# Optimization experiments

Measured on AMD Instinct MI355X. Metric: run time of the kernel, lower is better.

The kernel has to match this reference:

```python
import jax, jax.numpy as jnp
import numpy as np

D_MODEL = 1024
N_HEADS = 16
HEAD_DIM = D_MODEL // N_HEADS


def setup_inputs() -> dict:
    key = jax.random.key(0)
    k_x, k_q, k_k, k_v = jax.random.split(key, 4)
    B, S = 2, 2048
    x = jax.random.normal(k_x, (B, S, D_MODEL), dtype=jnp.float32)
    # nn.Linear weights stored as [out, in]; we apply x @ W.T
    scale = 1.0 / np.sqrt(D_MODEL)
    W_q = jax.random.uniform(k_q, (D_MODEL, D_MODEL), jnp.float32, -scale, scale)
    W_k = jax.random.uniform(k_k, (D_MODEL, D_MODEL), jnp.float32, -scale, scale)
    W_v = jax.random.uniform(k_v, (D_MODEL, D_MODEL), jnp.float32, -scale, scale)
    return {"x": x, "W_q": W_q, "W_k": W_k, "W_v": W_v}


def reference(x, W_q, W_k, W_v):
    B, S, D = x.shape
    H, Hd = N_HEADS, HEAD_DIM
    # QKV projections (Linear with no bias): x @ W.T
    Q = (x @ W_q.T).reshape(B, S, H, Hd).transpose(0, 2, 1, 3)  # [B,H,S,Hd]
    K = (x @ W_k.T).reshape(B, S, H, Hd).transpose(0, 2, 1, 3)
    V = (x @ W_v.T).reshape(B, S, H, Hd).transpose(0, 2, 1, 3)
    scores = jnp.einsum("bhqd,bhkd->bhqk", Q, K) / jnp.sqrt(jnp.float32(Hd))
    attn = jax.nn.softmax(scores, axis=-1)
    out = jnp.einsum("bhqk,bhkd->bhqd", attn, V)  # [B,H,S,Hd]
    return out.transpose(0, 2, 1, 3).reshape(B, S, H * Hd)
```

## Files before the change

kernel.cpp:

```cpp
#include <hip/hip_runtime.h>
#include <stdint.h>


typedef __bf16 bf16x8 __attribute__((ext_vector_type(8)));
typedef __bf16 bf16x4 __attribute__((ext_vector_type(4)));
typedef float  f32x4  __attribute__((ext_vector_type(4)));

#define D_MODEL 1024
#define SEQ     2048
#define NHEAD   16
#define HDIM    64
#define BS      4096

__device__ __forceinline__ void load_lds16(const void* g, void* lds) {
  __builtin_amdgcn_global_load_lds(
      (__attribute__((address_space(1))) void*)(uintptr_t)g,
      (__attribute__((address_space(3))) void*)(uintptr_t)lds,
      16, 0, 0);
}

#define NX4 1048576
#define NW4 262144
__global__ void cvt_all(const float* __restrict__ x,  const float* __restrict__ wq,
                        const float* __restrict__ wk, const float* __restrict__ wv,
                        __bf16* __restrict__ xb,  __bf16* __restrict__ wqb,
                        __bf16* __restrict__ wkb, __bf16* __restrict__ wvb) {
  int i = blockIdx.x * blockDim.x + threadIdx.x;
  const float* in; __bf16* out; int j;
  if (i < NX4)                { in = x;  out = xb;  j = i; }
  else if (i < NX4 + NW4)     { in = wq; out = wqb; j = i - NX4; }
  else if (i < NX4 + 2*NW4)   { in = wk; out = wkb; j = i - NX4 - NW4; }
  else                        { in = wv; out = wvb; j = i - NX4 - 2*NW4; }
  float4 v = ((const float4*)in)[j];
  bf16x4 o;
  o[0] = (__bf16)v.x; o[1] = (__bf16)v.y;
  o[2] = (__bf16)v.z; o[3] = (__bf16)v.w;
  ((bf16x4*)out)[j] = o;
}

__global__ __launch_bounds__(256) void qkv_gemm(
    const __bf16* __restrict__ X,
    const __bf16* __restrict__ Wq, const __bf16* __restrict__ Wk,
    const __bf16* __restrict__ Wv,
    __bf16* __restrict__ Qb, __bf16* __restrict__ Kb, __bf16* __restrict__ Vt) {
  __shared__ __bf16 As[128 * 32];
  __shared__ __bf16 Bs[128 * 32];

  const __bf16* W = (blockIdx.z == 0) ? Wq : (blockIdx.z == 1) ? Wk : Wv;

  const int t    = threadIdx.x;
  const int wv   = t >> 6;
  const int lane = t & 63;
  const int l15  = lane & 15;
  const int quad = lane >> 4;
  const int m0   = blockIdx.y * 128;
  const int n0   = blockIdx.x * 128;
  const int wm   = (wv >> 1) * 64;
  const int wn   = (wv & 1) * 64;

  f32x4 acc[4][4] = {};

  for (int it = 0; it < 32; ++it) {
    const int k0 = it * 32;
#pragma unroll
    for (int p = 0; p < 2; ++p) {
      const int c   = p * 256 + t;
      const int row = c >> 2;
      const int ko  = (c & 3) * 8;
      const unsigned lb = (unsigned)((p * 256 + wv * 64) * 16);
      load_lds16(X + (size_t)(m0 + row) * D_MODEL + k0 + ko, (char*)As + lb);
      load_lds16(W + (size_t)(n0 + row) * D_MODEL + k0 + ko, (char*)Bs + lb);
    }
    __syncthreads();

    bf16x8 af[4], bfb[4];
#pragma unroll
    for (int i = 0; i < 4; ++i)
      af[i] = *(const bf16x8*)&As[(wm + i * 16 + l15) * 32 + quad * 8];
#pragma unroll
    for (int j = 0; j < 4; ++j)
      bfb[j] = *(const bf16x8*)&Bs[(wn + j * 16 + l15) * 32 + quad * 8];
#pragma unroll
    for (int i = 0; i < 4; ++i)
#pragma unroll
      for (int j = 0; j < 4; ++j)
        acc[i][j] = __builtin_amdgcn_mfma_f32_16x16x32_bf16(af[i], bfb[j],
                                                            acc[i][j], 0, 0, 0);
    __syncthreads();
  }

  if (blockIdx.z != 2) {
    __bf16* Out = (blockIdx.z == 0) ? Qb : Kb;
    const float qs = (blockIdx.z == 0) ? 0.125f : 1.0f;
#pragma unroll
    for (int i = 0; i < 4; ++i) {
      const int rg = m0 + wm + i * 16 + quad * 4;
#pragma unroll
      for (int j = 0; j < 4; ++j) {
        const int cg = n0 + wn + j * 16 + l15;
#pragma unroll
        for (int r = 0; r < 4; ++r)
          Out[(size_t)(rg + r) * D_MODEL + cg] = (__bf16)(acc[i][j][r] * qs);
      }
    }
  } else {
#pragma unroll
    for (int i = 0; i < 4; ++i) {
      const int mg = m0 + wm + i * 16 + quad * 4;
#pragma unroll
      for (int j = 0; j < 4; ++j) {
        const int ng = n0 + wn + j * 16 + l15;
        bf16x4 v;
#pragma unroll
        for (int r = 0; r < 4; ++r) v[r] = (__bf16)acc[i][j][r];
        *(bf16x4*)&Vt[(size_t)ng * BS + mg] = v;
      }
    }
  }
}

__global__ __launch_bounds__(256) void attn(
    const __bf16* __restrict__ Qb, const __bf16* __restrict__ Kb,
    const __bf16* __restrict__ Vt, float* __restrict__ out) {
  __shared__ __bf16 Ks[64 * 64];
  __shared__ __bf16 Vs[64 * 64];
  __shared__ __bf16 Ps[4][32][72];

  const int t    = threadIdx.x;
  const int wv   = t >> 6;
  const int lane = t & 63;
  const int l15  = lane & 15;
  const int quad = lane >> 4;
  const int h    = blockIdx.y;
  const size_t bo = (size_t)blockIdx.z * SEQ;
  const int q0   = blockIdx.x * 128 + wv * 32;
  const int hd0  = h * HDIM;

  bf16x8 qf[2][2];
#pragma unroll
  for (int hh = 0; hh < 2; ++hh)
#pragma unroll
    for (int c = 0; c < 2; ++c)
      qf[hh][c] = *(const bf16x8*)&Qb[(bo + q0 + hh * 16 + l15) * D_MODEL +
                                      hd0 + c * 32 + quad * 8];

  float lsum[2][4] = {};
  f32x4 o_acc[2][4] = {};

  const int swz  = quad ^ (l15 & 7);
  const int swz4 = (quad + 4) ^ (l15 & 7);

  for (int kt = 0; kt < SEQ / 64; ++kt) {
    const int n0 = kt * 64;
#pragma unroll
    for (int p = 0; p < 2; ++p) {
      const int c   = p * 256 + t;
      const int row = c >> 3;
      const int cc  = (c & 7) ^ (row & 7);
      const unsigned lb = (unsigned)((p * 256 + wv * 64) * 16);
      load_lds16(Kb + (bo + n0 + row) * D_MODEL + hd0 + cc * 8, (char*)Ks + lb);
      load_lds16(Vt + (size_t)(hd0 + row) * BS + bo + n0 + cc * 8, (char*)Vs + lb);
    }
    __syncthreads();

    f32x4 s[2][4] = {};
#pragma unroll
    for (int nt = 0; nt < 4; ++nt) {
      const int r = nt * 16 + l15;
      bf16x8 kf0 = *(const bf16x8*)&Ks[(r * 8 + swz) * 8];
      bf16x8 kf1 = *(const bf16x8*)&Ks[(r * 8 + swz4) * 8];
#pragma unroll
      for (int hh = 0; hh < 2; ++hh) {
        s[hh][nt] = __builtin_amdgcn_mfma_f32_16x16x32_bf16(qf[hh][0], kf0, s[hh][nt], 0, 0, 0);
        s[hh][nt] = __builtin_amdgcn_mfma_f32_16x16x32_bf16(qf[hh][1], kf1, s[hh][nt], 0, 0, 0);
      }
    }

#pragma unroll
    for (int hh = 0; hh < 2; ++hh)
#pragma unroll
      for (int nt = 0; nt < 4; ++nt)
#pragma unroll
        for (int r = 0; r < 4; ++r) {
          float p = __expf(s[hh][nt][r]);
          lsum[hh][r] += p;
          Ps[wv][hh * 16 + quad * 4 + r][nt * 16 + l15] = (__bf16)p;
        }

#pragma unroll
    for (int tt = 0; tt < 4; ++tt) {
      const int r = tt * 16 + l15;
      bf16x8 vf0 = *(const bf16x8*)&Vs[(r * 8 + swz) * 8];
      bf16x8 vf1 = *(const bf16x8*)&Vs[(r * 8 + swz4) * 8];
#pragma unroll
      for (int hh = 0; hh < 2; ++hh) {
        bf16x8 pf0 = *(const bf16x8*)&Ps[wv][hh * 16 + l15][quad * 8];
        bf16x8 pf1 = *(const bf16x8*)&Ps[wv][hh * 16 + l15][32 + quad * 8];
        o_acc[hh][tt] = __builtin_amdgcn_mfma_f32_16x16x32_bf16(pf0, vf0, o_acc[hh][tt], 0, 0, 0);
        o_acc[hh][tt] = __builtin_amdgcn_mfma_f32_16x16x32_bf16(pf1, vf1, o_acc[hh][tt], 0, 0, 0);
      }
    }
    __syncthreads();
  }

#pragma unroll
  for (int hh = 0; hh < 2; ++hh)
#pragma unroll
    for (int r = 0; r < 4; ++r) {
      float s = lsum[hh][r];
      s += __shfl_xor(s, 1);
      s += __shfl_xor(s, 2);
      s += __shfl_xor(s, 4);
      s += __shfl_xor(s, 8);
      float inv = 1.f / s;
      const size_t row = bo + q0 + hh * 16 + quad * 4 + r;
#pragma unroll
      for (int tt = 0; tt < 4; ++tt)
        out[row * D_MODEL + hd0 + tt * 16 + l15] = o_acc[hh][tt][r] * inv;
    }
}

extern "C" void kernel_launch(void* const* d_in, const int* in_sizes, int n_in,
                              void* d_out, int out_size, void* d_ws, size_t ws_size,
                              hipStream_t stream) {
  const float* x  = (const float*)d_in[0];
  const float* Wq = (const float*)d_in[1];
  const float* Wk = (const float*)d_in[2];
  const float* Wv = (const float*)d_in[3];
  float* out = (float*)d_out;

  char* ws = (char*)d_ws;
  __bf16* xb  = (__bf16*)(ws);
  __bf16* wqb = (__bf16*)(ws + (8u  << 20));
  __bf16* wkb = (__bf16*)(ws + (10u << 20));
  __bf16* wvb = (__bf16*)(ws + (12u << 20));
  __bf16* Qbf = (__bf16*)(ws + (14u << 20));
  __bf16* Kbf = (__bf16*)(ws + (22u << 20));
  __bf16* Vt  = (__bf16*)(ws + (30u << 20));

  cvt_all<<<(NX4 + 3 * NW4) / 256, 256, 0, stream>>>(x, Wq, Wk, Wv,
                                                     xb, wqb, wkb, wvb);

  qkv_gemm<<<dim3(8, 32, 3), 256, 0, stream>>>(xb, wqb, wkb, wvb, Qbf, Kbf, Vt);

  attn<<<dim3(SEQ / 128, NHEAD, 2), 256, 0, stream>>>(Qbf, Kbf, Vt, out);
}
```

Baseline: 171.9 us.

## Keep P in registers via transposed 32x32 MFMA and permlane32 swap

Result: faster. 168.5 us (-2.0%).

```diff
diff --git a/kernel.cpp b/kernel.cpp
--- a/kernel.cpp
+++ b/kernel.cpp
@@ -5,6 +5,7 @@
 typedef __bf16 bf16x8 __attribute__((ext_vector_type(8)));
 typedef __bf16 bf16x4 __attribute__((ext_vector_type(4)));
 typedef float  f32x4  __attribute__((ext_vector_type(4)));
+typedef float  f32x16 __attribute__((ext_vector_type(16)));
 
 #define D_MODEL 1024
 #define SEQ     2048
@@ -124,31 +125,24 @@
     const __bf16* __restrict__ Vt, float* __restrict__ out) {
   __shared__ __bf16 Ks[64 * 64];
   __shared__ __bf16 Vs[64 * 64];
-  __shared__ __bf16 Ps[4][32][72];
 
   const int t    = threadIdx.x;
   const int wv   = t >> 6;
   const int lane = t & 63;
-  const int l15  = lane & 15;
-  const int quad = lane >> 4;
+  const int l31  = lane & 31;
+  const int half = lane >> 5;
   const int h    = blockIdx.y;
   const size_t bo = (size_t)blockIdx.z * SEQ;
   const int q0   = blockIdx.x * 128 + wv * 32;
   const int hd0  = h * HDIM;
 
-  bf16x8 qf[2][2];
-#pragma unroll
-  for (int hh = 0; hh < 2; ++hh)
-#pragma unroll
-    for (int c = 0; c < 2; ++c)
-      qf[hh][c] = *(const bf16x8*)&Qb[(bo + q0 + hh * 16 + l15) * D_MODEL +
-                                      hd0 + c * 32 + quad * 8];
-
-  float lsum[2][4] = {};
-  f32x4 o_acc[2][4] = {};
-
-  const int swz  = quad ^ (l15 & 7);
-  const int swz4 = (quad + 4) ^ (l15 & 7);
+  bf16x8 qf[4];
+#pragma unroll
+  for (int c = 0; c < 4; ++c)
+    qf[c] = *(const bf16x8*)&Qb[(bo + q0 + l31) * D_MODEL + hd0 + c * 16 + half * 8];
+
+  float lsum = 0.f;
+  f32x16 o_acc[2] = {};
 
   for (int kt = 0; kt < SEQ / 64; ++kt) {
     const int n0 = kt * 64;
@@ -163,60 +157,69 @@
     }
     __syncthreads();
 
-    f32x4 s[2][4] = {};
-#pragma unroll
-    for (int nt = 0; nt < 4; ++nt) {
-      const int r = nt * 16 + l15;
-      bf16x8 kf0 = *(const bf16x8*)&Ks[(r * 8 + swz) * 8];
-      bf16x8 kf1 = *(const bf16x8*)&Ks[(r * 8 + swz4) * 8];
-#pragma unroll
-      for (int hh = 0; hh < 2; ++hh) {
-        s[hh][nt] = __builtin_amdgcn_mfma_f32_16x16x32_bf16(qf[hh][0], kf0, s[hh][nt], 0, 0, 0);
-        s[hh][nt] = __builtin_amdgcn_mfma_f32_16x16x32_bf16(qf[hh][1], kf1, s[hh][nt], 0, 0, 0);
-      }
-    }
-
-#pragma unroll
-    for (int hh = 0; hh < 2; ++hh)
-#pragma unroll
-      for (int nt = 0; nt < 4; ++nt)
-#pragma unroll
-        for (int r = 0; r < 4; ++r) {
-          float p = __expf(s[hh][nt][r]);
-          lsum[hh][r] += p;
-          Ps[wv][hh * 16 + quad * 4 + r][nt * 16 + l15] = (__bf16)p;
+    f32x16 st[2];
+#pragma unroll
+    for (int ktile = 0; ktile < 2; ++ktile) {
+      f32x16 acc = {};
+      const int row = ktile * 32 + l31;
+#pragma unroll
+      for (int c = 0; c < 4; ++c) {
+        const int pc = (2 * c + half) ^ (row & 7);
+        bf16x8 kf = *(const bf16x8*)&Ks[(row * 8 + pc) * 8];
+        acc = __builtin_amdgcn_mfma_f32_32x32x16_bf16(kf, qf[c], acc, 0, 0, 0);
+      }
+      st[ktile] = acc;
+    }
+
+    uint32_t pk[2][8];
+#pragma unroll
+    for (int ktile = 0; ktile < 2; ++ktile)
+#pragma unroll
+      for (int i = 0; i < 8; ++i) {
+        float e0 = __expf(st[ktile][2 * i]);
+        float e1 = __expf(st[ktile][2 * i + 1]);
+        lsum += e0 + e1;
+        union { bf16x4 v; uint32_t u[2]; } pp;
+        pp.v[0] = (__bf16)e0; pp.v[1] = (__bf16)e1;
+        pk[ktile][i] = pp.u[0];
+      }
+
+#pragma unroll
+    for (int ktile = 0; ktile < 2; ++ktile)
+#pragma unroll
+      for (int kc = 0; kc < 2; ++kc) {
+        auto r02 = __builtin_amdgcn_permlane32_swap(pk[ktile][kc * 4 + 0],
+                                                    pk[ktile][kc * 4 + 2],
+                                                    false, false);
+        auto r13 = __builtin_amdgcn_permlane32_swap(pk[ktile][kc * 4 + 1],
+                                                    pk[ktile][kc * 4 + 3],
+                                                    false, false);
+        union { uint32_t u[4]; bf16x8 v; } pf;
+        pf.u[0] = r02[0]; pf.u[1] = r13[0];
+        pf.u[2] = r02[1]; pf.u[3] = r13[1];
+#pragma unroll
+        for (int dt = 0; dt < 2; ++dt) {
+          const int row = dt * 32 + l31;
+          const int pc  = (ktile * 4 + kc * 2 + half) ^ (row & 7);
+          bf16x8 vf = *(const bf16x8*)&Vs[(row * 8 + pc) * 8];
+          o_acc[dt] = __builtin_amdgcn_mfma_f32_32x32x16_bf16(vf, pf.v,
+                                                              o_acc[dt], 0, 0, 0);
         }
-
-#pragma unroll
-    for (int tt = 0; tt < 4; ++tt) {
-      const int r = tt * 16 + l15;
-      bf16x8 vf0 = *(const bf16x8*)&Vs[(r * 8 + swz) * 8];
-      bf16x8 vf1 = *(const bf16x8*)&Vs[(r * 8 + swz4) * 8];
-#pragma unroll
-      for (int hh = 0; hh < 2; ++hh) {
-        bf16x8 pf0 = *(const bf16x8*)&Ps[wv][hh * 16 + l15][quad * 8];
-        bf16x8 pf1 = *(const bf16x8*)&Ps[wv][hh * 16 + l15][32 + quad * 8];
-        o_acc[hh][tt] = __builtin_amdgcn_mfma_f32_16x16x32_bf16(pf0, vf0, o_acc[hh][tt], 0, 0, 0);
-        o_acc[hh][tt] = __builtin_amdgcn_mfma_f32_16x16x32_bf16(pf1, vf1, o_acc[hh][tt], 0, 0, 0);
-      }
-    }
+      }
     __syncthreads();
   }
 
-#pragma unroll
-  for (int hh = 0; hh < 2; ++hh)
-#pragma unroll
-    for (int r = 0; r < 4; ++r) {
-      float s = lsum[hh][r];
-      s += __shfl_xor(s, 1);
-      s += __shfl_xor(s, 2);
-      s += __shfl_xor(s, 4);
-      s += __shfl_xor(s, 8);
-      float inv = 1.f / s;
-      const size_t row = bo + q0 + hh * 16 + quad * 4 + r;
-#pragma unroll
-      for (int tt = 0; tt < 4; ++tt)
-        out[row * D_MODEL + hd0 + tt * 16 + l15] = o_acc[hh][tt][r] * inv;
+  lsum += __shfl_xor(lsum, 32);
+  const float inv = 1.f / lsum;
+
+  const size_t orow = (bo + q0 + l31) * D_MODEL + hd0;
+#pragma unroll
+  for (int dt = 0; dt < 2; ++dt)
+#pragma unroll
+    for (int g = 0; g < 4; ++g) {
+      float4 v = make_float4(o_acc[dt][4 * g + 0] * inv, o_acc[dt][4 * g + 1] * inv,
+                             o_acc[dt][4 * g + 2] * inv, o_acc[dt][4 * g + 3] * inv);
+      *(float4*)&out[orow + dt * 32 + g * 8 + half * 4] = v;
     }
 }
 
```
